# Optimization experiments

Measured on AMD Instinct MI355X. Metric: run time of the kernel, lower is better.

## Reference

```python
import jax, jax.numpy as jnp
import numpy as np

T_FRAMES = 16384
INPUT_DIM = 4096
N_PRED = 62
P = N_PRED + 2            # predicate_size incl START/STOP
START = P - 2
STOP = P - 1
NEG = -10000.0


def setup_inputs() -> dict:
    key = jax.random.key(0)
    k1, k2, k3, k4 = jax.random.split(key, 4)
    video = jax.random.normal(k1, (T_FRAMES, INPUT_DIM), dtype=jnp.float32)
    # hidden2predicate Linear(input_dim, P)
    W = jax.random.normal(k2, (P, INPUT_DIM), dtype=jnp.float32) * 0.02
    b = jax.random.normal(k3, (P,), dtype=jnp.float32) * 0.02
    # action_transitions: randn, with START row and STOP column clamped
    trans = jax.random.normal(k4, (P, P), dtype=jnp.float32)
    trans = trans.at[START, :].set(NEG)
    trans = trans.at[:, STOP].set(NEG)
    return {"video": video, "W": W, "b": b, "transitions": trans}


def reference(video, W, b, transitions):
    # emissions: ReLU(Linear(video))  -> [T, P]
    feats = jax.nn.relu(video @ W.T + b)

    # Viterbi decode (vectorized over tags, scan over time)
    init_fv = jnp.full((P,), NEG, dtype=feats.dtype).at[START].set(0.0)

    def step(fv, feat):
        # scores[next, prev] = fv[prev] + transitions[next, prev]
        scores = fv[None, :] + transitions
        bptr = jnp.argmax(scores, axis=1)           # [P] best prev per next
        fv_new = jnp.max(scores, axis=1) + feat     # [P]
        return fv_new, bptr

    fv, bptrs = jax.lax.scan(step, init_fv, feats)  # bptrs: [T, P]

    terminal = fv + transitions[STOP]
    best = jnp.argmax(terminal)
    path_score = terminal[best]

    # backtrace: emit tag at each step, carry its predecessor
    def back(tag, bp):
        return bp[tag], tag

    _, best_path = jax.lax.scan(back, best, bptrs, reverse=True)  # [T] int32
    return path_score, best_path
```

## Files before the change

kernel.cpp:

```cpp
#include <hip/hip_runtime.h>
#include <hip/hip_bf16.h>

#define T_FRAMES 16384
#define KDIM 4096
#define STARTS 62
#define STOPS 63
#define NEGV (-10000.0f)

#define CHUNK_L 16
#define BURN 48
#define NCHUNK (T_FRAMES / CHUNK_L)

#define BT_S 128
#define BT_C (T_FRAMES / BT_S)

typedef __attribute__((ext_vector_type(8))) short s16x8;
typedef __attribute__((ext_vector_type(4))) float f32x4;

__device__ __forceinline__ float lane_bcast(float v, int l) {
  return __uint_as_float(__builtin_amdgcn_readlane(__float_as_uint(v), l));
}

__device__ __forceinline__ unsigned short f2bf(float f) {
  unsigned u = __float_as_uint(f);
  return (unsigned short)((u + 0x7FFFu + ((u >> 16) & 1u)) >> 16);
}

__global__ __launch_bounds__(256) void wconv_kernel(
    const float* __restrict__ W, unsigned short* __restrict__ wbf) {
  int i = (blockIdx.x * 256 + threadIdx.x) * 4;
  float4 v = *(const float4*)&W[i];
  ushort4 o;
  o.x = f2bf(v.x); o.y = f2bf(v.y); o.z = f2bf(v.z); o.w = f2bf(v.w);
  *(ushort4*)&wbf[i] = o;
}

__global__ __launch_bounds__(256, 4) void gemm_mfma_kernel(
    const float* __restrict__ video, const unsigned short* __restrict__ wbf,
    const float* __restrict__ bias, float* __restrict__ feats) {
  __shared__ float red[4 * 16 * 68];
  const int tid = threadIdx.x;
  const int wave = tid >> 6, lane = tid & 63;
  const int col = lane & 15, quad = lane >> 4;
  const int m0 = blockIdx.x * 16;

  const float* aptr = video + (size_t)(m0 + col) * KDIM + quad * 8;
  const unsigned short* bptr0 = wbf + (size_t)col * KDIM + quad * 8;

  f32x4 acc[4];
#pragma unroll
  for (int nt = 0; nt < 4; ++nt) acc[nt] = (f32x4){0.f, 0.f, 0.f, 0.f};

  const int kbase = wave * (KDIM / 4);
#pragma unroll 2
  for (int kc = kbase; kc < kbase + KDIM / 4; kc += 32) {
    float4 a0 = *(const float4*)(aptr + kc);
    float4 a1 = *(const float4*)(aptr + kc + 4);
    s16x8 bf[4];
#pragma unroll
    for (int nt = 0; nt < 4; ++nt)
      bf[nt] = *(const s16x8*)(bptr0 + (size_t)nt * 16 * KDIM + kc);
    s16x8 af;
    af[0] = (short)f2bf(a0.x); af[1] = (short)f2bf(a0.y);
    af[2] = (short)f2bf(a0.z); af[3] = (short)f2bf(a0.w);
    af[4] = (short)f2bf(a1.x); af[5] = (short)f2bf(a1.y);
    af[6] = (short)f2bf(a1.z); af[7] = (short)f2bf(a1.w);
#pragma unroll
    for (int nt = 0; nt < 4; ++nt)
      acc[nt] = __builtin_amdgcn_mfma_f32_16x16x32_bf16(af, bf[nt], acc[nt], 0, 0, 0);
  }

#pragma unroll
  for (int nt = 0; nt < 4; ++nt)
#pragma unroll
    for (int r = 0; r < 4; ++r) {
      int m = quad * 4 + r, n = nt * 16 + col;
      red[wave * 1088 + m * 68 + n] = acc[nt][r];
    }
  __syncthreads();
  {
    int m = tid >> 4, n = (tid & 15) * 4;
    float4 s = *(const float4*)&red[0 * 1088 + m * 68 + n];
    float4 s1 = *(const float4*)&red[1 * 1088 + m * 68 + n];
    float4 s2 = *(const float4*)&red[2 * 1088 + m * 68 + n];
    float4 s3 = *(const float4*)&red[3 * 1088 + m * 68 + n];
    float4 bb = *(const float4*)&bias[n];
    float4 r;
    r.x = fmaxf(s.x + s1.x + s2.x + s3.x + bb.x, 0.f);
    r.y = fmaxf(s.y + s1.y + s2.y + s3.y + bb.y, 0.f);
    r.z = fmaxf(s.z + s1.z + s2.z + s3.z + bb.z, 0.f);
    r.w = fmaxf(s.w + s1.w + s2.w + s3.w + bb.w, 0.f);
    *(float4*)&feats[(size_t)(m0 + m) * 64 + n] = r;
  }
}

__global__ __launch_bounds__(64) void viterbi_fvbp_kernel(
    const float* __restrict__ feats, const float* __restrict__ trans,
    unsigned char* __restrict__ bptr, float* __restrict__ lastfv) {
  const int c = blockIdx.x;
  const int lane = threadIdx.x;
  float tr[64];
#pragma unroll
  for (int i = 0; i < 16; ++i) {
    float4 v = *(const float4*)&trans[lane * 64 + 4 * i];
    tr[4 * i + 0] = v.x;
    tr[4 * i + 1] = v.y;
    tr[4 * i + 2] = v.z;
    tr[4 * i + 3] = v.w;
  }
  const int rec0 = c * CHUNK_L;
  int t0 = rec0 - BURN;
  float fv;
  if (t0 <= 0) {
    t0 = 0;
    fv = (lane == STARTS) ? 0.0f : NEGV;
  } else {
    fv = 0.0f;
  }
  for (int t = t0; t < rec0; ++t) {
    float feat = feats[t * 64 + lane];
    float m0 = -3.0e38f, m1 = -3.0e38f, m2 = -3.0e38f, m3 = -3.0e38f;
#pragma unroll
    for (int p = 0; p < 64; p += 4) {
      m0 = fmaxf(m0, lane_bcast(fv, p + 0) + tr[p + 0]);
      m1 = fmaxf(m1, lane_bcast(fv, p + 1) + tr[p + 1]);
      m2 = fmaxf(m2, lane_bcast(fv, p + 2) + tr[p + 2]);
      m3 = fmaxf(m3, lane_bcast(fv, p + 3) + tr[p + 3]);
    }
    float nf = fmaxf(fmaxf(m0, m1), fmaxf(m2, m3)) + feat;
    nf = nf - lane_bcast(nf, 0);
    fv = nf;
  }
  for (int t = rec0; t < rec0 + CHUNK_L; ++t) {
    float feat = feats[t * 64 + lane];
    float m = -3.0e38f;
    int bi = 0;
#pragma unroll
    for (int p = 0; p < 64; ++p) {
      float s = lane_bcast(fv, p) + tr[p];
      if (s > m) { m = s; bi = p; }
    }
    bptr[t * 64 + lane] = (unsigned char)bi;
    float nf = m + feat;
    nf = nf - lane_bcast(nf, 0);
    if (t == T_FRAMES - 1) lastfv[lane] = nf;
    fv = nf;
  }
}

__global__ __launch_bounds__(128) void compose_kernel(
    const unsigned char* __restrict__ bptr, unsigned char* __restrict__ map8) {
  __shared__ unsigned char lb[BT_S * 64];
  __shared__ unsigned char sm[8 * 64];
  const int c = blockIdx.x, tid = threadIdx.x;
  const uint4* src = (const uint4*)(bptr + (size_t)c * BT_S * 64);
  uint4* dst = (uint4*)lb;
  for (int i = tid; i < (BT_S * 64) / 16; i += 128) dst[i] = src[i];
  __syncthreads();
  {
    const int st = tid & 63;
    const int sA = tid >> 6;
    int m0 = st, m1 = st, m2 = st, m3 = st;
#pragma unroll
    for (int i = 15; i >= 0; --i) {
      m0 = lb[((sA + 0) * 16 + i) * 64 + m0];
      m1 = lb[((sA + 2) * 16 + i) * 64 + m1];
      m2 = lb[((sA + 4) * 16 + i) * 64 + m2];
      m3 = lb[((sA + 6) * 16 + i) * 64 + m3];
    }
    sm[(sA + 0) * 64 + st] = (unsigned char)m0;
    sm[(sA + 2) * 64 + st] = (unsigned char)m1;
    sm[(sA + 4) * 64 + st] = (unsigned char)m2;
    sm[(sA + 6) * 64 + st] = (unsigned char)m3;
  }
  __syncthreads();
  if (tid < 64) {
    int m = tid;
#pragma unroll
    for (int s = 7; s >= 0; --s) m = sm[s * 64 + m];
    map8[c * 64 + tid] = (unsigned char)m;
  }
}

__global__ __launch_bounds__(128) void scan_kernel(
    const unsigned char* __restrict__ map8, const float* __restrict__ lastfv,
    const float* __restrict__ trans, int* __restrict__ enter,
    float* __restrict__ out0) {
  __shared__ unsigned char lm[BT_C * 64];
  __shared__ unsigned char sm[8 * 64];
  __shared__ int endt[8];
  __shared__ int sbest;
  const int tid = threadIdx.x;
  if (tid == 127) out0[0] = 0.0f;
  if (tid < 64) {
    float v = lastfv[tid] + trans[STOPS * 64 + tid];
    float m = -3.0e38f;
    int bi = 0;
#pragma unroll
    for (int p = 0; p < 64; ++p) {
      float s = lane_bcast(v, p);
      if (s > m) { m = s; bi = p; }
    }
    if (tid == 0) sbest = bi;
  }
  const uint4* src = (const uint4*)map8;
  uint4* dst = (uint4*)lm;
  for (int i = tid; i < (BT_C * 64) / 16; i += 128) dst[i] = src[i];
  __syncthreads();
  {
    const int st = tid & 63;
    const int sA = tid >> 6;
    int m0 = st, m1 = st, m2 = st, m3 = st;
#pragma unroll
    for (int i = 15; i >= 0; --i) {
      m0 = lm[((sA + 0) * 16 + i) * 64 + m0];
      m1 = lm[((sA + 2) * 16 + i) * 64 + m1];
      m2 = lm[((sA + 4) * 16 + i) * 64 + m2];
      m3 = lm[((sA + 6) * 16 + i) * 64 + m3];
    }
    sm[(sA + 0) * 64 + st] = (unsigned char)m0;
    sm[(sA + 2) * 64 + st] = (unsigned char)m1;
    sm[(sA + 4) * 64 + st] = (unsigned char)m2;
    sm[(sA + 6) * 64 + st] = (unsigned char)m3;
  }
  __syncthreads();
  if (tid == 0) {
    int e = sbest;
    endt[7] = e;
    for (int s = 7; s >= 1; --s) { e = sm[s * 64 + e]; endt[s - 1] = e; }
  }
  __syncthreads();
  if (tid < 8) {
    int e = endt[tid];
    for (int i = 15; i >= 0; --i) {
      int cc = tid * 16 + i;
      enter[cc] = e;
      e = lm[cc * 64 + e];
    }
  }
}

__global__ __launch_bounds__(128) void decode_score_kernel(
    const unsigned char* __restrict__ bptr, const int* __restrict__ enter,
    const float* __restrict__ feats, const float* __restrict__ trans,
    float* __restrict__ out) {
  __shared__ unsigned char lb[BT_S * 64];
  __shared__ unsigned char sm[8 * 64];
  __shared__ int endt[8];
  __shared__ unsigned char tl[BT_S];
  __shared__ double red[128];
  const int c = blockIdx.x, tid = threadIdx.x;
  const uint4* src = (const uint4*)(bptr + (size_t)c * BT_S * 64);
  uint4* dst = (uint4*)lb;
  for (int i = tid; i < (BT_S * 64) / 16; i += 128) dst[i] = src[i];
  __syncthreads();
  {
    const int st = tid & 63;
    const int sA = tid >> 6;
    int m0 = st, m1 = st, m2 = st, m3 = st;
#pragma unroll
    for (int i = 15; i >= 0; --i) {
      m0 = lb[((sA + 0) * 16 + i) * 64 + m0];
      m1 = lb[((sA + 2) * 16 + i) * 64 + m1];
      m2 = lb[((sA + 4) * 16 + i) * 64 + m2];
      m3 = lb[((sA + 6) * 16 + i) * 64 + m3];
    }
    sm[(sA + 0) * 64 + st] = (unsigned char)m0;
    sm[(sA + 2) * 64 + st] = (unsigned char)m1;
    sm[(sA + 4) * 64 + st] = (unsigned char)m2;
    sm[(sA + 6) * 64 + st] = (unsigned char)m3;
  }
  __syncthreads();
  if (tid == 0) {
    int e = enter[c];
    endt[7] = e;
    for (int s = 7; s >= 1; --s) { e = sm[s * 64 + e]; endt[s - 1] = e; }
  }
  __syncthreads();
  if (tid < 8) {
    int e = endt[tid];
    for (int i = 15; i >= 0; --i) {
      tl[tid * 16 + i] = (unsigned char)e;
      e = lb[(tid * 16 + i) * 64 + e];
    }
  }
  __syncthreads();
  const int t = c * BT_S + tid;
  const int tg = tl[tid];
  out[1 + t] = (float)tg;
  double sc = (double)feats[(size_t)t * 64 + tg];
  int prev = (tid == 0) ? ((c == 0) ? STARTS : enter[c - 1]) : (int)tl[tid - 1];
  sc += (double)trans[tg * 64 + prev];
  if (t == T_FRAMES - 1) sc += (double)trans[STOPS * 64 + tg];
  red[tid] = sc;
  __syncthreads();
  for (int off = 64; off > 0; off >>= 1) {
    if (tid < off) red[tid] += red[tid + off];
    __syncthreads();
  }
  if (tid == 0) atomicAdd(&out[0], (float)red[0]);
}

extern "C" void kernel_launch(void* const* d_in, const int* in_sizes, int n_in,
                              void* d_out, int out_size, void* d_ws,
                              size_t ws_size, hipStream_t stream) {
  const float* video = (const float*)d_in[0];
  const float* W = (const float*)d_in[1];
  const float* bias = (const float*)d_in[2];
  const float* trans = (const float*)d_in[3];
  float* out = (float*)d_out;

  char* ws = (char*)d_ws;
  float* feats = (float*)(ws);
  unsigned short* wbf = (unsigned short*)(ws + 0x400000);
  unsigned char* bptr = (unsigned char*)(ws + 0x500000);
  unsigned char* map8 = (unsigned char*)(ws + 0x600000);
  int* enter = (int*)(ws + 0x602000);
  float* lastfv = (float*)(ws + 0x603000);

  wconv_kernel<<<dim3(256), dim3(256), 0, stream>>>(W, wbf);
  gemm_mfma_kernel<<<dim3(T_FRAMES / 16), dim3(256), 0, stream>>>(video, wbf, bias, feats);
  viterbi_fvbp_kernel<<<dim3(NCHUNK), dim3(64), 0, stream>>>(feats, trans, bptr, lastfv);
  compose_kernel<<<dim3(BT_C), dim3(128), 0, stream>>>(bptr, map8);
  scan_kernel<<<dim3(1), dim3(128), 0, stream>>>(map8, lastfv, trans, enter, out);
  decode_score_kernel<<<dim3(BT_C), dim3(128), 0, stream>>>(bptr, enter, feats, trans, out);
}
```

Measured before the change: 469.9 us.

## Fuse GEMM with Viterbi chunks and merge backtrace kernels via flag sync

Each GEMM block now runs its own Viterbi chunk right after computing its 16 rows of emissions. It waits on per-chunk ready flags from earlier blocks for the burn-in rows, and the block order is permuted so dependencies finish earlier. The compose, scan and decode kernels are merged into one: the last block to arrive (tracked by an atomic counter) does the global scan, and the other blocks spin on a second flag. This removes launch overhead and the round-trip of emissions through global memory, but it relies on inter-block spin-waits that could stall or deadlock if the blocks are not co-resident. The argmax loop is also split into four independent chains.

```diff
diff --git a/kernel.cpp b/kernel.cpp
--- a/kernel.cpp
+++ b/kernel.cpp
@@ -1,5 +1,4 @@
 #include <hip/hip_runtime.h>
-#include <hip/hip_bf16.h>
 
 #define T_FRAMES 16384
 #define KDIM 4096
@@ -14,6 +13,8 @@
 #define BT_S 128
 #define BT_C (T_FRAMES / BT_S)
 
+#define SPIN_BOUND (1 << 20)
+
 typedef __attribute__((ext_vector_type(8))) short s16x8;
 typedef __attribute__((ext_vector_type(4))) float f32x4;
 
@@ -27,7 +28,11 @@
 }
 
 __global__ __launch_bounds__(256) void wconv_kernel(
-    const float* __restrict__ W, unsigned short* __restrict__ wbf) {
+    const float* __restrict__ W, unsigned short* __restrict__ wbf,
+    unsigned int* __restrict__ flags) {
+  if (blockIdx.x == 0) {
+    for (int j = threadIdx.x; j < NCHUNK + 2; j += 256) flags[j] = 0u;
+  }
   int i = (blockIdx.x * 256 + threadIdx.x) * 4;
   float4 v = *(const float4*)&W[i];
   ushort4 o;
@@ -35,14 +40,18 @@
   *(ushort4*)&wbf[i] = o;
 }
 
-__global__ __launch_bounds__(256, 4) void gemm_mfma_kernel(
+__global__ __launch_bounds__(256, 4) void gemm_vit_kernel(
     const float* __restrict__ video, const unsigned short* __restrict__ wbf,
-    const float* __restrict__ bias, float* __restrict__ feats) {
+    const float* __restrict__ bias, const float* __restrict__ trans,
+    float* __restrict__ feats, unsigned char* __restrict__ bptr,
+    float* __restrict__ lastfv, unsigned int* __restrict__ flags) {
   __shared__ float red[4 * 16 * 68];
+  __shared__ float fl[16 * 64];
   const int tid = threadIdx.x;
   const int wave = tid >> 6, lane = tid & 63;
   const int col = lane & 15, quad = lane >> 4;
-  const int m0 = blockIdx.x * 16;
+  const int c = ((blockIdx.x & 7) << 7) | (blockIdx.x >> 3);
+  const int m0 = c * 16;
 
   const float* aptr = video + (size_t)(m0 + col) * KDIM + quad * 8;
   const unsigned short* bptr0 = wbf + (size_t)col * KDIM + quad * 8;
@@ -91,14 +100,15 @@
     r.z = fmaxf(s.z + s1.z + s2.z + s3.z + bb.z, 0.f);
     r.w = fmaxf(s.w + s1.w + s2.w + s3.w + bb.w, 0.f);
     *(float4*)&feats[(size_t)(m0 + m) * 64 + n] = r;
-  }
-}
-
-__global__ __launch_bounds__(64) void viterbi_fvbp_kernel(
-    const float* __restrict__ feats, const float* __restrict__ trans,
-    unsigned char* __restrict__ bptr, float* __restrict__ lastfv) {
-  const int c = blockIdx.x;
-  const int lane = threadIdx.x;
+    *(float4*)&fl[m * 64 + n] = r;
+  }
+  __syncthreads();
+  if (tid == 0) {
+    __threadfence();
+    __hip_atomic_store(&flags[c], 1u, __ATOMIC_RELEASE, __HIP_MEMORY_SCOPE_AGENT);
+  }
+  if (wave != 0) return;
+
   float tr[64];
 #pragma unroll
   for (int i = 0; i < 16; ++i) {
@@ -108,7 +118,7 @@
     tr[4 * i + 2] = v.z;
     tr[4 * i + 3] = v.w;
   }
-  const int rec0 = c * CHUNK_L;
+  const int rec0 = m0;
   int t0 = rec0 - BURN;
   float fv;
   if (t0 <= 0) {
@@ -117,29 +127,49 @@
   } else {
     fv = 0.0f;
   }
-  for (int t = t0; t < rec0; ++t) {
-    float feat = feats[t * 64 + lane];
-    float m0 = -3.0e38f, m1 = -3.0e38f, m2 = -3.0e38f, m3 = -3.0e38f;
-#pragma unroll
-    for (int p = 0; p < 64; p += 4) {
-      m0 = fmaxf(m0, lane_bcast(fv, p + 0) + tr[p + 0]);
-      m1 = fmaxf(m1, lane_bcast(fv, p + 1) + tr[p + 1]);
-      m2 = fmaxf(m2, lane_bcast(fv, p + 2) + tr[p + 2]);
-      m3 = fmaxf(m3, lane_bcast(fv, p + 3) + tr[p + 3]);
-    }
-    float nf = fmaxf(fmaxf(m0, m1), fmaxf(m2, m3)) + feat;
-    nf = nf - lane_bcast(nf, 0);
-    fv = nf;
+  for (int tb = t0; tb < rec0; tb += 16) {
+    const int rb = tb >> 4;
+    int spins = 0;
+    while (__hip_atomic_load(&flags[rb], __ATOMIC_RELAXED,
+                             __HIP_MEMORY_SCOPE_AGENT) == 0u) {
+      __builtin_amdgcn_s_sleep(2);
+      if (++spins > SPIN_BOUND) break;
+    }
+    __threadfence();
+    for (int t = tb; t < tb + 16; ++t) {
+      float feat = feats[t * 64 + lane];
+      float q0 = -3.0e38f, q1 = -3.0e38f, q2 = -3.0e38f, q3 = -3.0e38f;
+#pragma unroll
+      for (int p = 0; p < 64; p += 4) {
+        q0 = fmaxf(q0, lane_bcast(fv, p + 0) + tr[p + 0]);
+        q1 = fmaxf(q1, lane_bcast(fv, p + 1) + tr[p + 1]);
+        q2 = fmaxf(q2, lane_bcast(fv, p + 2) + tr[p + 2]);
+        q3 = fmaxf(q3, lane_bcast(fv, p + 3) + tr[p + 3]);
+      }
+      float nf = fmaxf(fmaxf(q0, q1), fmaxf(q2, q3)) + feat;
+      nf = nf - lane_bcast(nf, 0);
+      fv = nf;
+    }
   }
   for (int t = rec0; t < rec0 + CHUNK_L; ++t) {
-    float feat = feats[t * 64 + lane];
-    float m = -3.0e38f;
-    int bi = 0;
-#pragma unroll
-    for (int p = 0; p < 64; ++p) {
-      float s = lane_bcast(fv, p) + tr[p];
-      if (s > m) { m = s; bi = p; }
-    }
+    float feat = fl[(t - rec0) * 64 + lane];
+    float g0 = -3.0e38f, g1 = -3.0e38f, g2 = -3.0e38f, g3 = -3.0e38f;
+    int b0 = 0, b1 = 16, b2 = 32, b3 = 48;
+#pragma unroll
+    for (int i = 0; i < 16; ++i) {
+      float s0 = lane_bcast(fv, i) + tr[i];
+      float s1 = lane_bcast(fv, i + 16) + tr[i + 16];
+      float s2 = lane_bcast(fv, i + 32) + tr[i + 32];
+      float s3 = lane_bcast(fv, i + 48) + tr[i + 48];
+      if (s0 > g0) { g0 = s0; b0 = i; }
+      if (s1 > g1) { g1 = s1; b1 = i + 16; }
+      if (s2 > g2) { g2 = s2; b2 = i + 32; }
+      if (s3 > g3) { g3 = s3; b3 = i + 48; }
+    }
+    float m = g0; int bi = b0;
+    if (g1 > m) { m = g1; bi = b1; }
+    if (g2 > m) { m = g2; bi = b2; }
+    if (g3 > m) { m = g3; bi = b3; }
     bptr[t * 64 + lane] = (unsigned char)bi;
     float nf = m + feat;
     nf = nf - lane_bcast(nf, 0);
@@ -148,14 +178,28 @@
   }
 }
 
-__global__ __launch_bounds__(128) void compose_kernel(
-    const unsigned char* __restrict__ bptr, unsigned char* __restrict__ map8) {
+__global__ __launch_bounds__(128) void backtrace_kernel(
+    const unsigned char* __restrict__ bptr, const float* __restrict__ feats,
+    const float* __restrict__ trans, const float* __restrict__ lastfv,
+    unsigned char* __restrict__ map8, int* __restrict__ enter,
+    unsigned int* __restrict__ cnt, unsigned int* __restrict__ flag2,
+    float* __restrict__ out) {
   __shared__ unsigned char lb[BT_S * 64];
   __shared__ unsigned char sm[8 * 64];
+  __shared__ unsigned char lm[BT_C * 64];
+  __shared__ unsigned char sm2[8 * 64];
+  __shared__ int endt[8];
+  __shared__ unsigned char tl[BT_S];
+  __shared__ double red[128];
+  __shared__ int sh_last;
+  __shared__ int sbest;
   const int c = blockIdx.x, tid = threadIdx.x;
-  const uint4* src = (const uint4*)(bptr + (size_t)c * BT_S * 64);
-  uint4* dst = (uint4*)lb;
-  for (int i = tid; i < (BT_S * 64) / 16; i += 128) dst[i] = src[i];
+
+  {
+    const uint4* src = (const uint4*)(bptr + (size_t)c * BT_S * 64);
+    uint4* dst = (uint4*)lb;
+    for (int i = tid; i < (BT_S * 64) / 16; i += 128) dst[i] = src[i];
+  }
   __syncthreads();
   {
     const int st = tid & 63;
@@ -180,95 +224,79 @@
     for (int s = 7; s >= 0; --s) m = sm[s * 64 + m];
     map8[c * 64 + tid] = (unsigned char)m;
   }
-}
-
-__global__ __launch_bounds__(128) void scan_kernel(
-    const unsigned char* __restrict__ map8, const float* __restrict__ lastfv,
-    const float* __restrict__ trans, int* __restrict__ enter,
-    float* __restrict__ out0) {
-  __shared__ unsigned char lm[BT_C * 64];
-  __shared__ unsigned char sm[8 * 64];
-  __shared__ int endt[8];
-  __shared__ int sbest;
-  const int tid = threadIdx.x;
-  if (tid == 127) out0[0] = 0.0f;
-  if (tid < 64) {
-    float v = lastfv[tid] + trans[STOPS * 64 + tid];
-    float m = -3.0e38f;
-    int bi = 0;
-#pragma unroll
-    for (int p = 0; p < 64; ++p) {
-      float s = lane_bcast(v, p);
-      if (s > m) { m = s; bi = p; }
-    }
-    if (tid == 0) sbest = bi;
-  }
-  const uint4* src = (const uint4*)map8;
-  uint4* dst = (uint4*)lm;
-  for (int i = tid; i < (BT_C * 64) / 16; i += 128) dst[i] = src[i];
-  __syncthreads();
-  {
-    const int st = tid & 63;
-    const int sA = tid >> 6;
-    int m0 = st, m1 = st, m2 = st, m3 = st;
-#pragma unroll
-    for (int i = 15; i >= 0; --i) {
-      m0 = lm[((sA + 0) * 16 + i) * 64 + m0];
-      m1 = lm[((sA + 2) * 16 + i) * 64 + m1];
-      m2 = lm[((sA + 4) * 16 + i) * 64 + m2];
-      m3 = lm[((sA + 6) * 16 + i) * 64 + m3];
-    }
-    sm[(sA + 0) * 64 + st] = (unsigned char)m0;
-    sm[(sA + 2) * 64 + st] = (unsigned char)m1;
-    sm[(sA + 4) * 64 + st] = (unsigned char)m2;
-    sm[(sA + 6) * 64 + st] = (unsigned char)m3;
-  }
   __syncthreads();
   if (tid == 0) {
-    int e = sbest;
-    endt[7] = e;
-    for (int s = 7; s >= 1; --s) { e = sm[s * 64 + e]; endt[s - 1] = e; }
-  }
-  __syncthreads();
-  if (tid < 8) {
-    int e = endt[tid];
-    for (int i = 15; i >= 0; --i) {
-      int cc = tid * 16 + i;
-      enter[cc] = e;
-      e = lm[cc * 64 + e];
-    }
-  }
-}
-
-__global__ __launch_bounds__(128) void decode_score_kernel(
-    const unsigned char* __restrict__ bptr, const int* __restrict__ enter,
-    const float* __restrict__ feats, const float* __restrict__ trans,
-    float* __restrict__ out) {
-  __shared__ unsigned char lb[BT_S * 64];
-  __shared__ unsigned char sm[8 * 64];
-  __shared__ int endt[8];
-  __shared__ unsigned char tl[BT_S];
-  __shared__ double red[128];
-  const int c = blockIdx.x, tid = threadIdx.x;
-  const uint4* src = (const uint4*)(bptr + (size_t)c * BT_S * 64);
-  uint4* dst = (uint4*)lb;
-  for (int i = tid; i < (BT_S * 64) / 16; i += 128) dst[i] = src[i];
-  __syncthreads();
-  {
-    const int st = tid & 63;
-    const int sA = tid >> 6;
-    int m0 = st, m1 = st, m2 = st, m3 = st;
-#pragma unroll
-    for (int i = 15; i >= 0; --i) {
-      m0 = lb[((sA + 0) * 16 + i) * 64 + m0];
-      m1 = lb[((sA + 2) * 16 + i) * 64 + m1];
-      m2 = lb[((sA + 4) * 16 + i) * 64 + m2];
-      m3 = lb[((sA + 6) * 16 + i) * 64 + m3];
-    }
-    sm[(sA + 0) * 64 + st] = (unsigned char)m0;
-    sm[(sA + 2) * 64 + st] = (unsigned char)m1;
-    sm[(sA + 4) * 64 + st] = (unsigned char)m2;
-    sm[(sA + 6) * 64 + st] = (unsigned char)m3;
+    __threadfence();
+    unsigned int old = atomicAdd(cnt, 1u);
+    sh_last = (old == (unsigned)(BT_C - 1)) ? 1 : 0;
+    if (sh_last) __threadfence();
+  }
+  __syncthreads();
+  if (sh_last) {
+    if (tid < 64) {
+      float v = lastfv[tid] + trans[STOPS * 64 + tid];
+      float m = -3.0e38f;
+      int bi = 0;
+#pragma unroll
+      for (int p = 0; p < 64; ++p) {
+        float s = lane_bcast(v, p);
+        if (s > m) { m = s; bi = p; }
+      }
+      if (tid == 0) sbest = bi;
+    }
+    {
+      const uint4* src = (const uint4*)map8;
+      uint4* dst = (uint4*)lm;
+      for (int i = tid; i < (BT_C * 64) / 16; i += 128) dst[i] = src[i];
+    }
+    __syncthreads();
+    {
+      const int st = tid & 63;
+      const int sA = tid >> 6;
+      int m0 = st, m1 = st, m2 = st, m3 = st;
+#pragma unroll
+      for (int i = 15; i >= 0; --i) {
+        m0 = lm[((sA + 0) * 16 + i) * 64 + m0];
+        m1 = lm[((sA + 2) * 16 + i) * 64 + m1];
+        m2 = lm[((sA + 4) * 16 + i) * 64 + m2];
+        m3 = lm[((sA + 6) * 16 + i) * 64 + m3];
+      }
+      sm2[(sA + 0) * 64 + st] = (unsigned char)m0;
+      sm2[(sA + 2) * 64 + st] = (unsigned char)m1;
+      sm2[(sA + 4) * 64 + st] = (unsigned char)m2;
+      sm2[(sA + 6) * 64 + st] = (unsigned char)m3;
+    }
+    __syncthreads();
+    if (tid == 0) {
+      int e = sbest;
+      endt[7] = e;
+      for (int s = 7; s >= 1; --s) { e = sm2[s * 64 + e]; endt[s - 1] = e; }
+    }
+    __syncthreads();
+    if (tid < 8) {
+      int e = endt[tid];
+      for (int i = 15; i >= 0; --i) {
+        int cc = tid * 16 + i;
+        enter[cc] = e;
+        e = lm[cc * 64 + e];
+      }
+    }
+    if (tid == 127) out[0] = 0.0f;
+    __syncthreads();
+    if (tid == 0) {
+      __threadfence();
+      __hip_atomic_store(flag2, 1u, __ATOMIC_RELEASE, __HIP_MEMORY_SCOPE_AGENT);
+    }
+  } else {
+    if (tid == 0) {
+      int spins = 0;
+      while (__hip_atomic_load(flag2, __ATOMIC_RELAXED,
+                               __HIP_MEMORY_SCOPE_AGENT) == 0u) {
+        __builtin_amdgcn_s_sleep(2);
+        if (++spins > SPIN_BOUND) break;
+      }
+      __threadfence();
+    }
   }
   __syncthreads();
   if (tid == 0) {
@@ -317,11 +345,12 @@
   unsigned char* map8 = (unsigned char*)(ws + 0x600000);
   int* enter = (int*)(ws + 0x602000);
   float* lastfv = (float*)(ws + 0x603000);
-
-  wconv_kernel<<<dim3(256), dim3(256), 0, stream>>>(W, wbf);
-  gemm_mfma_kernel<<<dim3(T_FRAMES / 16), dim3(256), 0, stream>>>(video, wbf, bias, feats);
-  viterbi_fvbp_kernel<<<dim3(NCHUNK), dim3(64), 0, stream>>>(feats, trans, bptr, lastfv);
-  compose_kernel<<<dim3(BT_C), dim3(128), 0, stream>>>(bptr, map8);
-  scan_kernel<<<dim3(1), dim3(128), 0, stream>>>(map8, lastfv, trans, enter, out);
-  decode_score_kernel<<<dim3(BT_C), dim3(128), 0, stream>>>(bptr, enter, feats, trans, out);
-}
+  unsigned int* flags = (unsigned int*)(ws + 0x604000);
+
+  wconv_kernel<<<dim3(256), dim3(256), 0, stream>>>(W, wbf, flags);
+  gemm_vit_kernel<<<dim3(NCHUNK), dim3(256), 0, stream>>>(
+      video, wbf, bias, trans, feats, bptr, lastfv, flags);
+  backtrace_kernel<<<dim3(BT_C), dim3(128), 0, stream>>>(
+      bptr, feats, trans, lastfv, map8, enter, flags + NCHUNK,
+      flags + NCHUNK + 1, out);
+}
```

After: 626.1 us. +33.2%, slower.
